# Optimization experiments

Hardware: AMD Instinct MI355X
Metric: run time of the kernel (lower is better)

Reference implementation:

```python
import jax, jax.numpy as jnp
import numpy as np

N = 50_000          # num_nodes
E = 800_000         # num_edges (avg degree 16)
DIMS = [512, 256, 256, 7]   # embedding_dim
SCALING = 2.0


def _glorot(key, shape):
    lim = float(np.sqrt(6.0 / (shape[0] + shape[1])))
    return jax.random.uniform(key, shape, jnp.float32, -lim, lim)


def setup_inputs() -> dict:
    key = jax.random.key(0)
    ks = jax.random.split(key, 16)
    inp = {
        "x": jax.random.normal(ks[0], (N, DIMS[0]), jnp.float32),
        "edge_index": jax.random.randint(ks[1], (2, E), 0, N, dtype=jnp.int32),
        # GCNConv weights (3 layers)
        "W1": _glorot(ks[2], (DIMS[0], DIMS[1])), "b1": jnp.zeros((DIMS[1],), jnp.float32),
        "W2": _glorot(ks[3], (DIMS[1], DIMS[2])), "b2": jnp.zeros((DIMS[2],), jnp.float32),
        "W3": _glorot(ks[4], (DIMS[2], DIMS[3])), "b3": jnp.zeros((DIMS[3],), jnp.float32),
        # pseudo_mlp: Linear(512,512) -> ReLU -> Linear(512,64) -> ReLU -> Linear(64,out)
        "mw1": _glorot(ks[5], (DIMS[0], 512)), "mb1": jnp.zeros((512,), jnp.float32),
        "mw2": _glorot(ks[6], (512, 64)),      "mb2": jnp.zeros((64,), jnp.float32),
        "mw3": _glorot(ks[7], (64, DIMS[-1])), "mb3": jnp.zeros((DIMS[-1],), jnp.float32),
        # parsing_mats[0] (only index 0 is used: learn_soft_edge3 always called with ln=0)
        "parsing0": jnp.ones((DIMS[-1], DIMS[-1]), jnp.float32) / SCALING,
    }
    return inp


def _gcn_conv(h_in, row, col, edge_weight, W, b):
    """PyG-style GCNConv with self-loops, symmetric norm, and per-edge weights."""
    h = h_in @ W                                  # [N, out]
    loop = jnp.arange(N, dtype=row.dtype)
    r = jnp.concatenate([row, loop])
    c = jnp.concatenate([col, loop])
    ew = jnp.concatenate([edge_weight, jnp.ones((N,), h.dtype)])
    deg = jax.ops.segment_sum(ew, c, num_segments=N)
    dinv = jnp.where(deg > 0, jax.lax.rsqrt(jnp.maximum(deg, 1e-12)), 0.0)
    norm = dinv[r] * ew * dinv[c]                 # [E+N]
    out = jax.ops.segment_sum(h[r] * norm[:, None], c, num_segments=N)
    return out + b


def _learn_soft_edge(x, row, col, mw1, mb1, mw2, mb2, mw3, mb3, parsing0):
    # pseudo_mlp logits
    h = jax.nn.relu(x @ mw1 + mb1)
    h = jax.nn.relu(h @ mw2 + mb2)
    logits = h @ mw3 + mb3                        # [N, C]
    s = logits[row]                               # start_logits [E, C]
    e = logits[col]                               # end_logits   [E, C]
    parsing = jax.nn.relu(SCALING * parsing0)     # [C, C]
    # diag(bmm(outer(s,e), P)).sum(-1) == sum_{c,d} s[e,c] * e[e,d] * P[d,c]
    ew = jnp.sum(s * (e @ parsing), axis=1)       # [E]
    mean = ew.mean()
    var = ew.var(ddof=1)                          # torch .var() is unbiased
    return (ew - mean) * jnp.sqrt(1e-4 / var) + 1.0


def reference(x, edge_index, W1, b1, W2, b2, W3, b3,
              mw1, mb1, mw2, mb2, mw3, mb3, parsing0):
    row, col = edge_index[0], edge_index[1]
    ew = _learn_soft_edge(x, row, col, mw1, mb1, mw2, mb2, mw3, mb3, parsing0)
    # layer 0
    h0 = _gcn_conv(x, row, col, ew, W1, b1)       # h = x (saved, pre-ReLU)
    x1 = jax.nn.relu(h0)                          # dropout is identity in eval
    # layer 1 (+ residual to h0)
    x2 = _gcn_conv(x1, row, col, ew, W2, b2)
    x2 = jax.nn.relu(x2) + h0
    # layer 2 (final, no activation)
    out = _gcn_conv(x2, row, col, ew, W3, b3)     # [N, n_classes]
    return out
```

## Files before the change

kernel.cpp:

```cpp
#include <hip/hip_runtime.h>

#define NN 50000
#define EE 800000
#define NB_EDGE 3125
#define NB_E1   1563
#define NB_SCAN 196

typedef __attribute__((ext_vector_type(4))) float f32x4;
typedef __attribute__((ext_vector_type(8))) short bf16x8;
typedef __attribute__((ext_vector_type(8))) unsigned short u16x8;

typedef const __attribute__((address_space(1))) void* gas_p;
typedef __attribute__((address_space(3))) void* las_p;

__device__ __forceinline__ float bf2f(unsigned short u) {
  union { unsigned int i; float f; } v; v.i = ((unsigned int)u) << 16; return v.f;
}
__device__ __forceinline__ unsigned short f2bf(float f) {
  union { float f; unsigned int i; } v; v.f = f;
  unsigned int u = v.i;
  return (unsigned short)((u + 0x7FFFu + ((u >> 16) & 1u)) >> 16);
}

__device__ __forceinline__ int xcd_swizzle(int orig, int nwg) {
  int xcd = orig & 7;
  int pos = orig >> 3;
  int q = nwg >> 3, r = nwg & 7;
  return (xcd < r ? xcd * (q + 1) : r * (q + 1) + (xcd - r) * q) + pos;
}

constexpr size_t O_XBF  = 0;
constexpr size_t O_H1   = O_XBF + 51200000;
constexpr size_t O_G1   = O_H1  + 51200000;
constexpr size_t O_X1   = O_G1  + 25600000;
constexpr size_t O_H2   = O_X1  + 25600000;
constexpr size_t O_LG   = O_H2  + 6400000;
constexpr size_t O_TG   = O_LG  + 1600000;
constexpr size_t O_EWR  = O_TG  + 1600000;
constexpr size_t O_W3P  = O_EWR + 3200000;
constexpr size_t O_RK   = O_W3P + 8192;
constexpr size_t O_CSR  = O_W3P + 3200000;
constexpr size_t O_MW1T = O_CSR + 6400000;
constexpr size_t O_W1T  = O_MW1T + 524288;
constexpr size_t O_W2T  = O_W1T  + 262144;
constexpr size_t O_MW2T = O_W2T  + 131072;
constexpr size_t O_CNT  = O_MW2T + 65536;
constexpr size_t O_RED  = O_CNT  + 200192;
constexpr size_t O_RPT  = O_RED  + 256;
constexpr size_t O_DINV = O_RPT  + 200192;
constexpr size_t O_BSUM = O_DINV + 200192;

__global__ __launch_bounds__(256) void conv_f2bf4(const float* __restrict__ in,
                                                  unsigned short* __restrict__ out, int n4) {
  int i = blockIdx.x * 256 + threadIdx.x;
  if (i >= n4) return;
  const float4 v = ((const float4*)in)[i];
  ushort4 o; o.x = f2bf(v.x); o.y = f2bf(v.y); o.z = f2bf(v.z); o.w = f2bf(v.w);
  ((ushort4*)out)[i] = o;
}

__global__ __launch_bounds__(256)
void conv_weights(const float* __restrict__ mw1, const float* __restrict__ W1,
                  const float* __restrict__ W2, const float* __restrict__ mw2,
                  const float* __restrict__ W3,
                  unsigned short* __restrict__ mw1t, unsigned short* __restrict__ w1t,
                  unsigned short* __restrict__ w2t, unsigned short* __restrict__ mw2t,
                  float* __restrict__ w3p)
{
  int i = blockIdx.x * 256 + threadIdx.x;
  if (i < 262144) {
    int k = i >> 9, n = i & 511;
    mw1t[(size_t)n * 512 + k] = f2bf(mw1[i]);
  } else if (i < 393216) {
    int j = i - 262144, k = j >> 8, n = j & 255;
    w1t[(size_t)n * 512 + k] = f2bf(W1[j]);
  } else if (i < 458752) {
    int j = i - 393216, k = j >> 8, n = j & 255;
    w2t[(size_t)n * 256 + k] = f2bf(W2[j]);
  } else if (i < 491520) {
    int j = i - 458752, k = j >> 6, n = j & 63;
    mw2t[(size_t)n * 512 + k] = f2bf(mw2[j]);
  } else if (i < 493568) {
    int j = i - 491520, d = j >> 3, c = j & 7;
    w3p[j] = (c < 7) ? W3[d * 7 + c] : 0.f;
  }
}

#define GEMM_STAGE(buf, k0)                                                        \
  _Pragma("unroll")                                                                \
  for (int r = 0; r < 4; ++r) {                                                    \
    const int row = r * 32 + wid * 8 + srow8;                                      \
    int ga = bm + row; ga = ga < M_ ? ga : M_ - 1;                                 \
    int gb = bn + row; gb = gb < N_ ? gb : N_ - 1;                                 \
    __builtin_amdgcn_global_load_lds((gas_p)(pA_ + ((size_t)ga * lda_ + (k0)) * 2 + sks * 16), \
                                     (las_p)(ldsA[buf] + row * 64), 16, 0, 0);     \
    __builtin_amdgcn_global_load_lds((gas_p)(pB_ + ((size_t)gb * ldb_ + (k0)) * 2 + sks * 16), \
                                     (las_p)(ldsB[buf] + row * 64), 16, 0, 0);     \
  }

#define GEMM_BODY(A, lda, Bt, ldb_K, M, Ncols, K, bm, bn)                          \
  __shared__ unsigned short ldsA[2][128 * 64];                                     \
  __shared__ unsigned short ldsB[2][128 * 64];                                     \
  const char* pA_ = (const char*)(A);                                              \
  const char* pB_ = (const char*)(Bt);                                             \
  const int lda_ = (lda), ldb_ = (ldb_K), M_ = (M), N_ = (Ncols);                  \
  const int tid  = threadIdx.x;                                                    \
  const int lane = tid & 63;                                                       \
  const int wid  = tid >> 6;                                                       \
  const int wm   = (wid >> 1) << 6;                                                \
  const int wn   = (wid & 1) << 6;                                                 \
  f32x4 acc[4][4] = {};                                                            \
  const int srow8 = lane >> 3;                                                     \
  const int sks   = (lane & 7) ^ srow8;                                            \
  const int nt    = (K) >> 6;                                                      \
  GEMM_STAGE(0, 0)                                                                 \
  for (int t = 0; t < nt; ++t) {                                                   \
    const int cur = t & 1;                                                         \
    if (t + 1 < nt) {                                                              \
      GEMM_STAGE(cur ^ 1, (t + 1) << 6)                                            \
      asm volatile("s_waitcnt vmcnt(8)" ::: "memory");                             \
    } else {                                                                       \
      asm volatile("s_waitcnt vmcnt(0)" ::: "memory");                             \
    }                                                                              \
    __builtin_amdgcn_s_barrier();                                                  \
    __builtin_amdgcn_sched_barrier(0);                                             \
    const int q   = lane >> 4;                                                     \
    const int r15 = lane & 15;                                                     \
    _Pragma("unroll")                                                              \
    for (int kk = 0; kk < 2; ++kk) {                                               \
      bf16x8 af[4], bfr[4];                                                        \
      _Pragma("unroll")                                                            \
      for (int m = 0; m < 4; ++m) {                                                \
        const int ra = wm + m * 16 + r15;                                          \
        af[m]  = *(const bf16x8*)(ldsA[cur] + ra * 64 + (((kk << 2) + q) ^ (ra & 7)) * 8); \
        const int rb = wn + m * 16 + r15;                                          \
        bfr[m] = *(const bf16x8*)(ldsB[cur] + rb * 64 + (((kk << 2) + q) ^ (rb & 7)) * 8); \
      }                                                                            \
      _Pragma("unroll")                                                            \
      for (int m = 0; m < 4; ++m)                                                  \
        _Pragma("unroll")                                                          \
        for (int n = 0; n < 4; ++n)                                                \
          acc[m][n] = __builtin_amdgcn_mfma_f32_16x16x32_bf16(af[m], bfr[n], acc[m][n], 0, 0, 0); \
    }                                                                              \
    __builtin_amdgcn_sched_barrier(0);                                             \
    __builtin_amdgcn_s_barrier();                                                  \
  }

template<bool RELU, bool BIAS>
__global__ __launch_bounds__(256)
void gemm_bf16(const unsigned short* __restrict__ A, int lda,
               const unsigned short* __restrict__ Bt,
               const float* __restrict__ bias,
               unsigned short* __restrict__ C, int ldc,
               int M, int N, int K)
{
  const int nwg  = gridDim.x * gridDim.y;
  const int wgid = xcd_swizzle(blockIdx.y * gridDim.x + blockIdx.x, nwg);
  const int bn   = (wgid % gridDim.x) << 7;
  const int bm   = (wgid / gridDim.x) << 7;

  GEMM_BODY(A, lda, Bt, K, M, N, K, bm, bn)

  const int q   = lane >> 4;
  const int r15 = lane & 15;
#pragma unroll
  for (int m = 0; m < 4; ++m) {
#pragma unroll
    for (int n = 0; n < 4; ++n) {
      const int gc = bn + wn + n * 16 + r15;
#pragma unroll
      for (int i = 0; i < 4; ++i) {
        const int gr = bm + wm + m * 16 + q * 4 + i;
        if (gr < M && gc < N) {
          float f = acc[m][n][i];
          if (BIAS) f += bias[gc];
          if (RELU) f = fmaxf(f, 0.f);
          C[(size_t)gr * ldc + gc] = f2bf(f);
        }
      }
    }
  }
}

__global__ __launch_bounds__(256)
void gemm_fused(const unsigned short* __restrict__ A,
                const unsigned short* __restrict__ Bt,
                const float* __restrict__ mb1,
                unsigned short* __restrict__ h1,
                unsigned short* __restrict__ g1,
                int M)
{
  const int nwg  = gridDim.x * gridDim.y;
  const int wgid = xcd_swizzle(blockIdx.y * gridDim.x + blockIdx.x, nwg);
  const int bnt  = wgid % gridDim.x;
  const int bn   = bnt << 7;
  const int bm   = (wgid / gridDim.x) << 7;

  GEMM_BODY(A, 512, Bt, 512, M, 768, 512, bm, bn)

  const int q   = lane >> 4;
  const int r15 = lane & 15;
  if (bnt < 4) {
#pragma unroll
    for (int m = 0; m < 4; ++m) {
#pragma unroll
      for (int n = 0; n < 4; ++n) {
        const int gc = bn + wn + n * 16 + r15;
        const float b = mb1[gc];
#pragma unroll
        for (int i = 0; i < 4; ++i) {
          const int gr = bm + wm + m * 16 + q * 4 + i;
          if (gr < M) h1[(size_t)gr * 512 + gc] = f2bf(fmaxf(acc[m][n][i] + b, 0.f));
        }
      }
    }
  } else {
#pragma unroll
    for (int m = 0; m < 4; ++m) {
#pragma unroll
      for (int n = 0; n < 4; ++n) {
        const int gc = bn - 512 + wn + n * 16 + r15;
#pragma unroll
        for (int i = 0; i < 4; ++i) {
          const int gr = bm + wm + m * 16 + q * 4 + i;
          if (gr < M) g1[(size_t)gr * 256 + gc] = f2bf(acc[m][n][i]);
        }
      }
    }
  }
}

__global__ __launch_bounds__(256)
void logits_kernel(const unsigned short* __restrict__ h2, const float* __restrict__ mw3,
                   const float* __restrict__ mb3, const float* __restrict__ par,
                   float* __restrict__ Lg, float* __restrict__ Tg)
{
  __shared__ float w[64 * 8];
  __shared__ float P[64];
  int tid = threadIdx.x;
  for (int i = tid; i < 512; i += 256) {
    int k = i >> 3, c = i & 7;
    w[i] = (c < 7) ? mw3[k * 7 + c] : 0.f;
  }
  if (tid < 64) {
    int d = tid >> 3, c = tid & 7;
    P[tid] = (d < 7 && c < 7) ? fmaxf(2.0f * par[d * 7 + c], 0.f) : 0.f;
  }
  __syncthreads();
  int n = blockIdx.x * 256 + tid;
  if (n >= NN) return;
  const unsigned short* hr = h2 + (size_t)n * 64;
  f32x4 L0 = {0,0,0,0}, L1 = {0,0,0,0};
  for (int k = 0; k < 64; k += 4) {
    ushort4 v = *(const ushort4*)(hr + k);
    float xs[4] = {bf2f(v.x), bf2f(v.y), bf2f(v.z), bf2f(v.w)};
#pragma unroll
    for (int j = 0; j < 4; ++j) {
      L0 += xs[j] * *(const f32x4*)&w[(k + j) * 8];
      L1 += xs[j] * *(const f32x4*)&w[(k + j) * 8 + 4];
    }
  }
  float Ls[8] = {L0[0], L0[1], L0[2], L0[3], L1[0], L1[1], L1[2], 0.f};
#pragma unroll
  for (int c = 0; c < 7; ++c) Ls[c] += mb3[c];
  f32x4 T0 = {0,0,0,0}, T1 = {0,0,0,0};
#pragma unroll
  for (int d = 0; d < 7; ++d) {
    T0 += Ls[d] * *(const f32x4*)&P[d * 8];
    T1 += Ls[d] * *(const f32x4*)&P[d * 8 + 4];
  }
  f32x4 o0 = {Ls[0], Ls[1], Ls[2], Ls[3]};
  f32x4 o1 = {Ls[4], Ls[5], Ls[6], 0.f};
  *(f32x4*)(Lg + (size_t)n * 8)     = o0;
  *(f32x4*)(Lg + (size_t)n * 8 + 4) = o1;
  *(f32x4*)(Tg + (size_t)n * 8)     = T0;
  *(f32x4*)(Tg + (size_t)n * 8 + 4) = T1;
}

__global__ __launch_bounds__(256)
void edge1_kernel(const int* __restrict__ row, const int* __restrict__ col,
                  const float* __restrict__ Lg, const float* __restrict__ Tg,
                  float* __restrict__ ew_raw, int* __restrict__ cnt,
                  unsigned short* __restrict__ rk, double* __restrict__ part)
{
  __shared__ double shs[4], shs2[4];
  const int e0 = blockIdx.x * 512 + threadIdx.x;
  const int e1 = e0 + 256;
  double s = 0.0, s2 = 0.0;
  if (e1 < EE) {
    int r0 = row[e0], c0 = col[e0];
    int r1 = row[e1], c1 = col[e1];
    float4 a00 = *(const float4*)(Lg + (size_t)r0 * 8);
    float4 a01 = *(const float4*)(Lg + (size_t)r0 * 8 + 4);
    float4 a10 = *(const float4*)(Lg + (size_t)r1 * 8);
    float4 a11 = *(const float4*)(Lg + (size_t)r1 * 8 + 4);
    float4 b00 = *(const float4*)(Tg + (size_t)c0 * 8);
    float4 b01 = *(const float4*)(Tg + (size_t)c0 * 8 + 4);
    float4 b10 = *(const float4*)(Tg + (size_t)c1 * 8);
    float4 b11 = *(const float4*)(Tg + (size_t)c1 * 8 + 4);
    float v0 = a00.x*b00.x + a00.y*b00.y + a00.z*b00.z + a00.w*b00.w
             + a01.x*b01.x + a01.y*b01.y + a01.z*b01.z + a01.w*b01.w;
    float v1 = a10.x*b10.x + a10.y*b10.y + a10.z*b10.z + a10.w*b10.w
             + a11.x*b11.x + a11.y*b11.y + a11.z*b11.z + a11.w*b11.w;
    ew_raw[e0] = v0; ew_raw[e1] = v1;
    int p0 = atomicAdd(&cnt[c0], 1);
    int p1 = atomicAdd(&cnt[c1], 1);
    rk[e0] = (unsigned short)p0;
    rk[e1] = (unsigned short)p1;
    s = (double)v0 + (double)v1;
    s2 = (double)v0 * (double)v0 + (double)v1 * (double)v1;
  } else if (e0 < EE) {
    int r0 = row[e0], c0 = col[e0];
    float4 a00 = *(const float4*)(Lg + (size_t)r0 * 8);
    float4 a01 = *(const float4*)(Lg + (size_t)r0 * 8 + 4);
    float4 b00 = *(const float4*)(Tg + (size_t)c0 * 8);
    float4 b01 = *(const float4*)(Tg + (size_t)c0 * 8 + 4);
    float v0 = a00.x*b00.x + a00.y*b00.y + a00.z*b00.z + a00.w*b00.w
             + a01.x*b01.x + a01.y*b01.y + a01.z*b01.z + a01.w*b01.w;
    ew_raw[e0] = v0;
    int p0 = atomicAdd(&cnt[c0], 1);
    rk[e0] = (unsigned short)p0;
    s = (double)v0; s2 = (double)v0 * (double)v0;
  }
  for (int off = 32; off; off >>= 1) {
    s  += __shfl_down(s, off);
    s2 += __shfl_down(s2, off);
  }
  int wv = threadIdx.x >> 6;
  if ((threadIdx.x & 63) == 0) { shs[wv] = s; shs2[wv] = s2; }
  __syncthreads();
  if (threadIdx.x == 0) {
    part[blockIdx.x]         = shs[0] + shs[1] + shs[2] + shs[3];
    part[NB_E1 + blockIdx.x] = shs2[0] + shs2[1] + shs2[2] + shs2[3];
  }
}

__global__ __launch_bounds__(1024)
void redpart_kernel(const double* __restrict__ part, double* __restrict__ red)
{
  __shared__ double sh[16][2];
  int tid = threadIdx.x;
  double s = 0.0, s2 = 0.0;
  for (int i = tid; i < NB_E1; i += 1024) {
    s  += part[i];
    s2 += part[NB_E1 + i];
  }
  for (int off = 32; off; off >>= 1) {
    s  += __shfl_down(s, off);
    s2 += __shfl_down(s2, off);
  }
  if ((tid & 63) == 0) { sh[tid >> 6][0] = s; sh[tid >> 6][1] = s2; }
  __syncthreads();
  if (tid == 0) {
    double a = 0.0, b = 0.0;
    for (int i = 0; i < 16; ++i) { a += sh[i][0]; b += sh[i][1]; }
    red[0] = a; red[1] = b;
  }
}

__global__ __launch_bounds__(256)
void edge2_kernel(const int* __restrict__ row, const int* __restrict__ col,
                  const float* __restrict__ ew_raw, const unsigned short* __restrict__ rk,
                  const double* __restrict__ red, const int* __restrict__ rowptr,
                  int2* __restrict__ csr_sw)
{
  int e = blockIdx.x * 256 + threadIdx.x;
  if (e >= EE) return;
  double mean = red[0] / (double)EE;
  double var  = (red[1] - (double)EE * mean * mean) / (double)(EE - 1);
  double scl  = sqrt(1e-4 / var);
  float v = (float)(((double)ew_raw[e] - mean) * scl) + 1.0f;
  int r = row[e], c = col[e];
  int2 sw; sw.x = r; sw.y = __float_as_int(v);
  csr_sw[rowptr[c] + (int)rk[e]] = sw;
}

__global__ __launch_bounds__(256)
void degdinv_kernel(const int* __restrict__ rowptr, const int2* __restrict__ csr_sw,
                    float* __restrict__ dinv)
{
  int n = blockIdx.x * 256 + threadIdx.x;
  if (n >= NN) return;
  int s = rowptr[n], e = rowptr[n + 1];
  float deg = 0.f;
  for (int i = s; i < e; ++i) deg += __int_as_float(csr_sw[i].y);
  float d = deg + 1.0f;
  dinv[n] = d > 0.f ? 1.0f / sqrtf(fmaxf(d, 1e-12f)) : 0.f;
}

__global__ __launch_bounds__(256)
void scale_csr_kernel(int2* __restrict__ csr_sw, const float* __restrict__ dinv)
{
  int i = blockIdx.x * 256 + threadIdx.x;
  if (i >= EE) return;
  int2 sw = csr_sw[i];
  sw.y = __float_as_int(__int_as_float(sw.y) * dinv[sw.x]);
  csr_sw[i] = sw;
}

__global__ __launch_bounds__(256)
void scan1_kernel(const int* __restrict__ cnt, int* __restrict__ bsum)
{
  __shared__ int sh[4];
  int i = blockIdx.x * 256 + threadIdx.x;
  int v = (i < NN) ? cnt[i] : 0;
  for (int off = 32; off; off >>= 1) v += __shfl_down(v, off);
  if ((threadIdx.x & 63) == 0) sh[threadIdx.x >> 6] = v;
  __syncthreads();
  if (threadIdx.x == 0) bsum[blockIdx.x] = sh[0] + sh[1] + sh[2] + sh[3];
}

__global__ __launch_bounds__(256)
void scan2_kernel(int* __restrict__ bsum)
{
  __shared__ int sh[256];
  int tid = threadIdx.x;
  int v = (tid < NB_SCAN) ? bsum[tid] : 0;
  sh[tid] = v;
  __syncthreads();
  for (int off = 1; off < 256; off <<= 1) {
    int t = (tid >= off) ? sh[tid - off] : 0;
    __syncthreads();
    sh[tid] += t;
    __syncthreads();
  }
  if (tid < NB_SCAN) bsum[tid] = sh[tid] - v;
}

__global__ __launch_bounds__(256)
void scan3_kernel(const int* __restrict__ cnt, const int* __restrict__ bsum,
                  int* __restrict__ rowptr)
{
  __shared__ int sh[256];
  int tid = threadIdx.x;
  int i = blockIdx.x * 256 + tid;
  int v = (i < NN) ? cnt[i] : 0;
  sh[tid] = v;
  __syncthreads();
  for (int off = 1; off < 256; off <<= 1) {
    int t = (tid >= off) ? sh[tid - off] : 0;
    __syncthreads();
    sh[tid] += t;
    __syncthreads();
  }
  if (i < NN) rowptr[i + 1] = bsum[blockIdx.x] + sh[tid];
  if (i == 0) rowptr[0] = 0;
}

#define AGG_ACC(sw_, v_)                                                     \
  {                                                                          \
    float w_ = __int_as_float((sw_).y);                                      \
    a0 += w_ * bf2f((v_)[0]); a1 += w_ * bf2f((v_)[1]);                      \
    a2 += w_ * bf2f((v_)[2]); a3 += w_ * bf2f((v_)[3]);                      \
    a4 += w_ * bf2f((v_)[4]); a5 += w_ * bf2f((v_)[5]);                      \
    a6 += w_ * bf2f((v_)[6]); a7 += w_ * bf2f((v_)[7]);                      \
  }

template<int MODE>
__global__ __launch_bounds__(256)
void agg256_kernel(const int* __restrict__ rowptr, const int2* __restrict__ csr_sw,
                   const unsigned short* __restrict__ gsrc,
                   const float* __restrict__ dinv, const float* __restrict__ bias,
                   const unsigned short* __restrict__ h0in,
                   unsigned short* __restrict__ h0out,
                   unsigned short* __restrict__ xout,
                   const float* __restrict__ w3p, float* __restrict__ y3)
{
  const int tid = threadIdx.x;
  const int hw  = tid >> 5;
  const int l5  = tid & 31;
  const size_t colbase = (size_t)(l5 << 3);
  const int stride = (int)gridDim.x * 8;

  for (int n = blockIdx.x * 8 + hw; n < NN; n += stride) {
    const int dbase = l5 << 3;
    const float dn = dinv[n];
    u16x8 sv = *(const u16x8*)(gsrc + (size_t)n * 256 + dbase);
    float4 b0 = *(const float4*)(bias + dbase);
    float4 b1 = *(const float4*)(bias + dbase + 4);
    float a0=0,a1=0,a2=0,a3=0,a4=0,a5=0,a6=0,a7=0;
    const int s = rowptr[n], e = rowptr[n + 1];
    int i = s;
    for (; i + 7 < e; i += 8) {
      int2 sw[8];
#pragma unroll
      for (int u = 0; u < 8; ++u) sw[u] = csr_sw[i + u];
      u16x8 v[8];
#pragma unroll
      for (int u = 0; u < 8; ++u) v[u] = *(const u16x8*)(gsrc + (size_t)sw[u].x * 256 + colbase);
#pragma unroll
      for (int u = 0; u < 8; ++u) AGG_ACC(sw[u], v[u])
    }
    for (; i + 3 < e; i += 4) {
      int2 sw[4];
#pragma unroll
      for (int u = 0; u < 4; ++u) sw[u] = csr_sw[i + u];
      u16x8 v[4];
#pragma unroll
      for (int u = 0; u < 4; ++u) v[u] = *(const u16x8*)(gsrc + (size_t)sw[u].x * 256 + colbase);
#pragma unroll
      for (int u = 0; u < 4; ++u) AGG_ACC(sw[u], v[u])
    }
    for (; i < e; ++i) {
      int2 sw = csr_sw[i];
      u16x8 v = *(const u16x8*)(gsrc + (size_t)sw.x * 256 + colbase);
      AGG_ACC(sw, v)
    }
    const float wd = dn * dn;
    float f0 = dn * a0 + wd * bf2f(sv[0]) + b0.x;
    float f1 = dn * a1 + wd * bf2f(sv[1]) + b0.y;
    float f2 = dn * a2 + wd * bf2f(sv[2]) + b0.z;
    float f3 = dn * a3 + wd * bf2f(sv[3]) + b0.w;
    float f4 = dn * a4 + wd * bf2f(sv[4]) + b1.x;
    float f5 = dn * a5 + wd * bf2f(sv[5]) + b1.y;
    float f6 = dn * a6 + wd * bf2f(sv[6]) + b1.z;
    float f7 = dn * a7 + wd * bf2f(sv[7]) + b1.w;
    const size_t o = (size_t)n * 256 + dbase;
    if (MODE == 0) {
      u16x8 h;
      h[0] = f2bf(f0); h[1] = f2bf(f1); h[2] = f2bf(f2); h[3] = f2bf(f3);
      h[4] = f2bf(f4); h[5] = f2bf(f5); h[6] = f2bf(f6); h[7] = f2bf(f7);
      *(u16x8*)(h0out + o) = h;
      u16x8 xo;
      xo[0] = f2bf(fmaxf(f0, 0.f)); xo[1] = f2bf(fmaxf(f1, 0.f));
      xo[2] = f2bf(fmaxf(f2, 0.f)); xo[3] = f2bf(fmaxf(f3, 0.f));
      xo[4] = f2bf(fmaxf(f4, 0.f)); xo[5] = f2bf(fmaxf(f5, 0.f));
      xo[6] = f2bf(fmaxf(f6, 0.f)); xo[7] = f2bf(fmaxf(f7, 0.f));
      *(u16x8*)(xout + o) = xo;
    } else {
      u16x8 h = *(const u16x8*)(h0in + o);
      float xv0 = bf2f(f2bf(fmaxf(f0, 0.f) + bf2f(h[0])));
      float xv1 = bf2f(f2bf(fmaxf(f1, 0.f) + bf2f(h[1])));
      float xv2 = bf2f(f2bf(fmaxf(f2, 0.f) + bf2f(h[2])));
      float xv3 = bf2f(f2bf(fmaxf(f3, 0.f) + bf2f(h[3])));
      float xv4 = bf2f(f2bf(fmaxf(f4, 0.f) + bf2f(h[4])));
      float xv5 = bf2f(f2bf(fmaxf(f5, 0.f) + bf2f(h[5])));
      float xv6 = bf2f(f2bf(fmaxf(f6, 0.f) + bf2f(h[6])));
      float xv7 = bf2f(f2bf(fmaxf(f7, 0.f) + bf2f(h[7])));
      const float* w3r = w3p + (size_t)dbase * 8;
      f32x4 p0 = {0,0,0,0}, p1 = {0,0,0,0};
      p0 += xv0 * *(const f32x4*)(w3r +  0); p1 += xv0 * *(const f32x4*)(w3r +  4);
      p0 += xv1 * *(const f32x4*)(w3r +  8); p1 += xv1 * *(const f32x4*)(w3r + 12);
      p0 += xv2 * *(const f32x4*)(w3r + 16); p1 += xv2 * *(const f32x4*)(w3r + 20);
      p0 += xv3 * *(const f32x4*)(w3r + 24); p1 += xv3 * *(const f32x4*)(w3r + 28);
      p0 += xv4 * *(const f32x4*)(w3r + 32); p1 += xv4 * *(const f32x4*)(w3r + 36);
      p0 += xv5 * *(const f32x4*)(w3r + 40); p1 += xv5 * *(const f32x4*)(w3r + 44);
      p0 += xv6 * *(const f32x4*)(w3r + 48); p1 += xv6 * *(const f32x4*)(w3r + 52);
      p0 += xv7 * *(const f32x4*)(w3r + 56); p1 += xv7 * *(const f32x4*)(w3r + 60);
#pragma unroll
      for (int off = 1; off < 32; off <<= 1) {
        p0[0] += __shfl_xor(p0[0], off); p0[1] += __shfl_xor(p0[1], off);
        p0[2] += __shfl_xor(p0[2], off); p0[3] += __shfl_xor(p0[3], off);
        p1[0] += __shfl_xor(p1[0], off); p1[1] += __shfl_xor(p1[1], off);
        p1[2] += __shfl_xor(p1[2], off); p1[3] += __shfl_xor(p1[3], off);
      }
      if (l5 == 0) {
        *(f32x4*)(y3 + (size_t)n * 8)     = p0;
        *(f32x4*)(y3 + (size_t)n * 8 + 4) = p1;
      }
    }
  }
}

__global__ __launch_bounds__(256)
void agg7_kernel(const int* __restrict__ rowptr, const int2* __restrict__ csr_sw,
                 const float* __restrict__ y3,
                 const float* __restrict__ dinv, const float* __restrict__ b3,
                 float* __restrict__ out)
{
  int n = blockIdx.x * 32 + (threadIdx.x >> 3);
  if (n >= NN) return;
  int j = threadIdx.x & 7;
  float acc = 0.f;
  int s = rowptr[n], e = rowptr[n + 1];
  int i = s;
  for (; i + 3 < e; i += 4) {
    int2 sw0 = csr_sw[i],     sw1 = csr_sw[i + 1];
    int2 sw2 = csr_sw[i + 2], sw3 = csr_sw[i + 3];
    float v0 = y3[(size_t)sw0.x * 8 + j];
    float v1 = y3[(size_t)sw1.x * 8 + j];
    float v2 = y3[(size_t)sw2.x * 8 + j];
    float v3 = y3[(size_t)sw3.x * 8 + j];
    acc += __int_as_float(sw0.y) * v0 + __int_as_float(sw1.y) * v1
         + __int_as_float(sw2.y) * v2 + __int_as_float(sw3.y) * v3;
  }
  for (; i < e; ++i) {
    int2 sw = csr_sw[i];
    acc += __int_as_float(sw.y) * y3[(size_t)sw.x * 8 + j];
  }
  float dn = dinv[n];
  acc = dn * acc + dn * dn * y3[(size_t)n * 8 + j];
  if (j < 7) out[(size_t)n * 7 + j] = acc + b3[j];
}

extern "C" void kernel_launch(void* const* d_in, const int* in_sizes, int n_in,
                              void* d_out, int out_size, void* d_ws, size_t ws_size,
                              hipStream_t stream)
{
  const float* x   = (const float*)d_in[0];
  const int*   ei  = (const int*)d_in[1];
  const float* W1  = (const float*)d_in[2];
  const float* b1  = (const float*)d_in[3];
  const float* W2  = (const float*)d_in[4];
  const float* b2  = (const float*)d_in[5];
  const float* W3  = (const float*)d_in[6];
  const float* b3  = (const float*)d_in[7];
  const float* mw1 = (const float*)d_in[8];
  const float* mb1 = (const float*)d_in[9];
  const float* mw2 = (const float*)d_in[10];
  const float* mb2 = (const float*)d_in[11];
  const float* mw3 = (const float*)d_in[12];
  const float* mb3 = (const float*)d_in[13];
  const float* par = (const float*)d_in[14];
  const int* row = ei;
  const int* col = ei + EE;
  float* out = (float*)d_out;

  char* ws = (char*)d_ws;
  unsigned short* x_bf  = (unsigned short*)(ws + O_XBF);
  unsigned short* h0    = (unsigned short*)(ws + O_XBF);
  unsigned short* h1_bf = (unsigned short*)(ws + O_H1);
  unsigned short* g2_bf = (unsigned short*)(ws + O_H1);
  unsigned short* g1_bf = (unsigned short*)(ws + O_G1);
  unsigned short* x1_bf = (unsigned short*)(ws + O_X1);
  unsigned short* h2_bf = (unsigned short*)(ws + O_H2);
  float* Lg      = (float*)(ws + O_LG);
  float* Tg      = (float*)(ws + O_TG);
  float* ew_raw  = (float*)(ws + O_EWR);
  float* y3      = (float*)(ws + O_EWR);
  float* w3p     = (float*)(ws + O_W3P);
  unsigned short* rk = (unsigned short*)(ws + O_RK);
  int2*  csr_sw  = (int2*)(ws + O_CSR);
  double* part   = (double*)(ws + O_CSR);
  unsigned short* mw1t = (unsigned short*)(ws + O_MW1T);
  unsigned short* w1t  = (unsigned short*)(ws + O_W1T);
  unsigned short* w2t  = (unsigned short*)(ws + O_W2T);
  unsigned short* mw2t = (unsigned short*)(ws + O_MW2T);
  int*    cnt    = (int*)(ws + O_CNT);
  double* red    = (double*)(ws + O_RED);
  int*    rowptr = (int*)(ws + O_RPT);
  float*  dinv   = (float*)(ws + O_DINV);
  int*    bsum   = (int*)(ws + O_BSUM);

  hipMemsetAsync(ws + O_CNT, 0, 200192, stream);

  conv_f2bf4<<<25000, 256, 0, stream>>>(x, x_bf, NN * 512 / 4);
  conv_weights<<<1929, 256, 0, stream>>>(mw1, W1, W2, mw2, W3, mw1t, w1t, w2t, mw2t, w3p);

  gemm_fused<<<dim3(6, 391), 256, 0, stream>>>(x_bf, mw1t, mb1, h1_bf, g1_bf, NN);
  gemm_bf16<true,  true ><<<dim3(1, 391), 256, 0, stream>>>(h1_bf, 512, mw2t, mb2, h2_bf, 64, NN, 64, 512);
  logits_kernel<<<196, 256, 0, stream>>>(h2_bf, mw3, mb3, par, Lg, Tg);

  edge1_kernel<<<NB_E1, 256, 0, stream>>>(row, col, Lg, Tg, ew_raw, cnt, rk, part);
  redpart_kernel<<<1, 1024, 0, stream>>>(part, red);
  scan1_kernel<<<NB_SCAN, 256, 0, stream>>>(cnt, bsum);
  scan2_kernel<<<1, 256, 0, stream>>>(bsum);
  scan3_kernel<<<NB_SCAN, 256, 0, stream>>>(cnt, bsum, rowptr);
  edge2_kernel<<<NB_EDGE, 256, 0, stream>>>(row, col, ew_raw, rk, red, rowptr, csr_sw);
  degdinv_kernel<<<196, 256, 0, stream>>>(rowptr, csr_sw, dinv);
  scale_csr_kernel<<<NB_EDGE, 256, 0, stream>>>(csr_sw, dinv);

  agg256_kernel<0><<<1536, 256, 0, stream>>>(rowptr, csr_sw, g1_bf, dinv, b1, nullptr, h0, x1_bf, nullptr, nullptr);
  gemm_bf16<false, false><<<dim3(2, 391), 256, 0, stream>>>(x1_bf, 256, w2t, nullptr, g2_bf, 256, NN, 256, 256);
  agg256_kernel<1><<<1536, 256, 0, stream>>>(rowptr, csr_sw, g2_bf, dinv, b2, h0, nullptr, nullptr, w3p, y3);
  agg7_kernel<<<1563, 256, 0, stream>>>(rowptr, csr_sw, y3, dinv, b3, out);
}
```

Measured before the change: 377.2 us.

## Fuse MLP second GEMM with logits projection and widen edge1 per-thread work

Replaces the separate 512->64 GEMM and the logits kernel with one MFMA kernel that computes the 64-wide hidden layer in registers, then applies ReLU, the 64->7 projection with a lane shuffle reduction, and the parsing-matrix transform before writing Lg/Tg. This removes the h2 round trip through global memory and one launch. Separately, edge1 now processes four edges per thread with the gathers batched, so fewer blocks are launched and more loads are in flight per thread. The 128x64 tile with 2x4 MFMA per wave gives small per-block work and more shuffle reductions in the epilogue.

```diff
diff --git a/kernel.cpp b/kernel.cpp
--- a/kernel.cpp
+++ b/kernel.cpp
@@ -3,7 +3,7 @@
 #define NN 50000
 #define EE 800000
 #define NB_EDGE 3125
-#define NB_E1   1563
+#define NB_E1   782
 #define NB_SCAN 196
 
 typedef __attribute__((ext_vector_type(4))) float f32x4;
@@ -39,6 +39,7 @@
 constexpr size_t O_EWR  = O_TG  + 1600000;
 constexpr size_t O_W3P  = O_EWR + 3200000;
 constexpr size_t O_RK   = O_W3P + 8192;
+constexpr size_t O_MW3P = O_RK  + 1600000;
 constexpr size_t O_CSR  = O_W3P + 3200000;
 constexpr size_t O_MW1T = O_CSR + 6400000;
 constexpr size_t O_W1T  = O_MW1T + 524288;
@@ -62,10 +63,10 @@
 __global__ __launch_bounds__(256)
 void conv_weights(const float* __restrict__ mw1, const float* __restrict__ W1,
                   const float* __restrict__ W2, const float* __restrict__ mw2,
-                  const float* __restrict__ W3,
+                  const float* __restrict__ W3, const float* __restrict__ mw3,
                   unsigned short* __restrict__ mw1t, unsigned short* __restrict__ w1t,
                   unsigned short* __restrict__ w2t, unsigned short* __restrict__ mw2t,
-                  float* __restrict__ w3p)
+                  float* __restrict__ w3p, float* __restrict__ mw3p)
 {
   int i = blockIdx.x * 256 + threadIdx.x;
   if (i < 262144) {
@@ -83,6 +84,9 @@
   } else if (i < 493568) {
     int j = i - 491520, d = j >> 3, c = j & 7;
     w3p[j] = (c < 7) ? W3[d * 7 + c] : 0.f;
+  } else if (i < 494080) {
+    int j = i - 493568, d = j >> 3, c = j & 7;
+    mw3p[j] = (c < 7) ? mw3[d * 7 + c] : 0.f;
   }
 }
 
@@ -231,50 +235,127 @@
 }
 
 __global__ __launch_bounds__(256)
-void logits_kernel(const unsigned short* __restrict__ h2, const float* __restrict__ mw3,
-                   const float* __restrict__ mb3, const float* __restrict__ par,
-                   float* __restrict__ Lg, float* __restrict__ Tg)
-{
-  __shared__ float w[64 * 8];
-  __shared__ float P[64];
-  int tid = threadIdx.x;
-  for (int i = tid; i < 512; i += 256) {
-    int k = i >> 3, c = i & 7;
-    w[i] = (c < 7) ? mw3[k * 7 + c] : 0.f;
-  }
+void mlp2_logits_kernel(const unsigned short* __restrict__ A,
+                        const unsigned short* __restrict__ Bt,
+                        const float* __restrict__ mb2,
+                        const float* __restrict__ mw3p,
+                        const float* __restrict__ mb3,
+                        const float* __restrict__ par,
+                        float* __restrict__ Lg, float* __restrict__ Tg,
+                        int M)
+{
+  __shared__ unsigned short ldsA[2][128 * 64];
+  __shared__ unsigned short ldsB[2][64 * 64];
+  __shared__ float Psh[64];
+  const int tid  = threadIdx.x;
+  const int lane = tid & 63;
+  const int wid  = tid >> 6;
+  const int bm   = blockIdx.x << 7;
+  f32x4 acc[2][4] = {};
+  const int srow8 = lane >> 3;
+  const int sks   = (lane & 7) ^ srow8;
+
   if (tid < 64) {
     int d = tid >> 3, c = tid & 7;
-    P[tid] = (d < 7 && c < 7) ? fmaxf(2.0f * par[d * 7 + c], 0.f) : 0.f;
-  }
-  __syncthreads();
-  int n = blockIdx.x * 256 + tid;
-  if (n >= NN) return;
-  const unsigned short* hr = h2 + (size_t)n * 64;
-  f32x4 L0 = {0,0,0,0}, L1 = {0,0,0,0};
-  for (int k = 0; k < 64; k += 4) {
-    ushort4 v = *(const ushort4*)(hr + k);
-    float xs[4] = {bf2f(v.x), bf2f(v.y), bf2f(v.z), bf2f(v.w)};
-#pragma unroll
-    for (int j = 0; j < 4; ++j) {
-      L0 += xs[j] * *(const f32x4*)&w[(k + j) * 8];
-      L1 += xs[j] * *(const f32x4*)&w[(k + j) * 8 + 4];
-    }
-  }
-  float Ls[8] = {L0[0], L0[1], L0[2], L0[3], L1[0], L1[1], L1[2], 0.f};
-#pragma unroll
-  for (int c = 0; c < 7; ++c) Ls[c] += mb3[c];
-  f32x4 T0 = {0,0,0,0}, T1 = {0,0,0,0};
-#pragma unroll
-  for (int d = 0; d < 7; ++d) {
-    T0 += Ls[d] * *(const f32x4*)&P[d * 8];
-    T1 += Ls[d] * *(const f32x4*)&P[d * 8 + 4];
-  }
-  f32x4 o0 = {Ls[0], Ls[1], Ls[2], Ls[3]};
-  f32x4 o1 = {Ls[4], Ls[5], Ls[6], 0.f};
-  *(f32x4*)(Lg + (size_t)n * 8)     = o0;
-  *(f32x4*)(Lg + (size_t)n * 8 + 4) = o1;
-  *(f32x4*)(Tg + (size_t)n * 8)     = T0;
-  *(f32x4*)(Tg + (size_t)n * 8 + 4) = T1;
+    Psh[tid] = (d < 7 && c < 7) ? fmaxf(2.0f * par[d * 7 + c], 0.f) : 0.f;
+  }
+
+#define M2_STAGE(buf, k0)                                                          \
+  _Pragma("unroll")                                                                \
+  for (int r = 0; r < 4; ++r) {                                                    \
+    const int rowA = r * 32 + wid * 8 + srow8;                                     \
+    int ga = bm + rowA; ga = ga < M ? ga : M - 1;                                  \
+    __builtin_amdgcn_global_load_lds((gas_p)((const char*)A + ((size_t)ga * 512 + (k0)) * 2 + sks * 16), \
+                                     (las_p)(ldsA[buf] + rowA * 64), 16, 0, 0);    \
+  }                                                                                \
+  _Pragma("unroll")                                                                \
+  for (int r = 0; r < 2; ++r) {                                                    \
+    const int rowB = r * 32 + wid * 8 + srow8;                                     \
+    __builtin_amdgcn_global_load_lds((gas_p)((const char*)Bt + ((size_t)rowB * 512 + (k0)) * 2 + sks * 16), \
+                                     (las_p)(ldsB[buf] + rowB * 64), 16, 0, 0);    \
+  }
+
+  M2_STAGE(0, 0)
+  for (int t = 0; t < 8; ++t) {
+    const int cur = t & 1;
+    if (t < 7) {
+      M2_STAGE(cur ^ 1, (t + 1) << 6)
+      asm volatile("s_waitcnt vmcnt(6)" ::: "memory");
+    } else {
+      asm volatile("s_waitcnt vmcnt(0)" ::: "memory");
+    }
+    __builtin_amdgcn_s_barrier();
+    __builtin_amdgcn_sched_barrier(0);
+    const int q   = lane >> 4;
+    const int r15 = lane & 15;
+#pragma unroll
+    for (int kk = 0; kk < 2; ++kk) {
+      bf16x8 af[2], bfr[4];
+#pragma unroll
+      for (int m = 0; m < 2; ++m) {
+        const int ra = wid * 32 + m * 16 + r15;
+        af[m] = *(const bf16x8*)(ldsA[cur] + ra * 64 + (((kk << 2) + q) ^ (ra & 7)) * 8);
+      }
+#pragma unroll
+      for (int n = 0; n < 4; ++n) {
+        const int rb = n * 16 + r15;
+        bfr[n] = *(const bf16x8*)(ldsB[cur] + rb * 64 + (((kk << 2) + q) ^ (rb & 7)) * 8);
+      }
+#pragma unroll
+      for (int m = 0; m < 2; ++m)
+#pragma unroll
+        for (int n = 0; n < 4; ++n)
+          acc[m][n] = __builtin_amdgcn_mfma_f32_16x16x32_bf16(af[m], bfr[n], acc[m][n], 0, 0, 0);
+    }
+    __builtin_amdgcn_sched_barrier(0);
+    __builtin_amdgcn_s_barrier();
+  }
+
+  const int q   = lane >> 4;
+  const int r15 = lane & 15;
+#pragma unroll
+  for (int m = 0; m < 2; ++m) {
+#pragma unroll
+    for (int i = 0; i < 4; ++i) {
+      f32x4 Llo = {0,0,0,0}, Lhi = {0,0,0,0};
+#pragma unroll
+      for (int n = 0; n < 4; ++n) {
+        const int colB = n * 16 + r15;
+        float h2v = fmaxf(acc[m][n][i] + mb2[colB], 0.f);
+        Llo += h2v * *(const f32x4*)(mw3p + colB * 8);
+        Lhi += h2v * *(const f32x4*)(mw3p + colB * 8 + 4);
+      }
+#pragma unroll
+      for (int off = 1; off < 16; off <<= 1) {
+        Llo[0] += __shfl_xor(Llo[0], off); Llo[1] += __shfl_xor(Llo[1], off);
+        Llo[2] += __shfl_xor(Llo[2], off); Llo[3] += __shfl_xor(Llo[3], off);
+        Lhi[0] += __shfl_xor(Lhi[0], off); Lhi[1] += __shfl_xor(Lhi[1], off);
+        Lhi[2] += __shfl_xor(Lhi[2], off); Lhi[3] += __shfl_xor(Lhi[3], off);
+      }
+      if (r15 == 0) {
+        const int grow = bm + wid * 32 + m * 16 + q * 4 + i;
+        if (grow < M) {
+          float Ls[8];
+          Ls[0] = Llo[0] + mb3[0]; Ls[1] = Llo[1] + mb3[1];
+          Ls[2] = Llo[2] + mb3[2]; Ls[3] = Llo[3] + mb3[3];
+          Ls[4] = Lhi[0] + mb3[4]; Ls[5] = Lhi[1] + mb3[5];
+          Ls[6] = Lhi[2] + mb3[6]; Ls[7] = 0.f;
+          f32x4 T0 = {0,0,0,0}, T1 = {0,0,0,0};
+#pragma unroll
+          for (int d = 0; d < 7; ++d) {
+            T0 += Ls[d] * *(const f32x4*)&Psh[d * 8];
+            T1 += Ls[d] * *(const f32x4*)&Psh[d * 8 + 4];
+          }
+          f32x4 o0 = {Ls[0], Ls[1], Ls[2], Ls[3]};
+          f32x4 o1 = {Ls[4], Ls[5], Ls[6], 0.f};
+          *(f32x4*)(Lg + (size_t)grow * 8)     = o0;
+          *(f32x4*)(Lg + (size_t)grow * 8 + 4) = o1;
+          *(f32x4*)(Tg + (size_t)grow * 8)     = T0;
+          *(f32x4*)(Tg + (size_t)grow * 8 + 4) = T1;
+        }
+      }
+    }
+  }
 }
 
 __global__ __launch_bounds__(256)
@@ -284,43 +365,30 @@
                   unsigned short* __restrict__ rk, double* __restrict__ part)
 {
   __shared__ double shs[4], shs2[4];
-  const int e0 = blockIdx.x * 512 + threadIdx.x;
-  const int e1 = e0 + 256;
+  const int base = blockIdx.x * 1024 + threadIdx.x;
   double s = 0.0, s2 = 0.0;
-  if (e1 < EE) {
-    int r0 = row[e0], c0 = col[e0];
-    int r1 = row[e1], c1 = col[e1];
-    float4 a00 = *(const float4*)(Lg + (size_t)r0 * 8);
-    float4 a01 = *(const float4*)(Lg + (size_t)r0 * 8 + 4);
-    float4 a10 = *(const float4*)(Lg + (size_t)r1 * 8);
-    float4 a11 = *(const float4*)(Lg + (size_t)r1 * 8 + 4);
-    float4 b00 = *(const float4*)(Tg + (size_t)c0 * 8);
-    float4 b01 = *(const float4*)(Tg + (size_t)c0 * 8 + 4);
-    float4 b10 = *(const float4*)(Tg + (size_t)c1 * 8);
-    float4 b11 = *(const float4*)(Tg + (size_t)c1 * 8 + 4);
-    float v0 = a00.x*b00.x + a00.y*b00.y + a00.z*b00.z + a00.w*b00.w
-             + a01.x*b01.x + a01.y*b01.y + a01.z*b01.z + a01.w*b01.w;
-    float v1 = a10.x*b10.x + a10.y*b10.y + a10.z*b10.z + a10.w*b10.w
-             + a11.x*b11.x + a11.y*b11.y + a11.z*b11.z + a11.w*b11.w;
-    ew_raw[e0] = v0; ew_raw[e1] = v1;
-    int p0 = atomicAdd(&cnt[c0], 1);
-    int p1 = atomicAdd(&cnt[c1], 1);
-    rk[e0] = (unsigned short)p0;
-    rk[e1] = (unsigned short)p1;
-    s = (double)v0 + (double)v1;
-    s2 = (double)v0 * (double)v0 + (double)v1 * (double)v1;
-  } else if (e0 < EE) {
-    int r0 = row[e0], c0 = col[e0];
-    float4 a00 = *(const float4*)(Lg + (size_t)r0 * 8);
-    float4 a01 = *(const float4*)(Lg + (size_t)r0 * 8 + 4);
-    float4 b00 = *(const float4*)(Tg + (size_t)c0 * 8);
-    float4 b01 = *(const float4*)(Tg + (size_t)c0 * 8 + 4);
-    float v0 = a00.x*b00.x + a00.y*b00.y + a00.z*b00.z + a00.w*b00.w
-             + a01.x*b01.x + a01.y*b01.y + a01.z*b01.z + a01.w*b01.w;
-    ew_raw[e0] = v0;
-    int p0 = atomicAdd(&cnt[c0], 1);
-    rk[e0] = (unsigned short)p0;
-    s = (double)v0; s2 = (double)v0 * (double)v0;
+  int idx[4]; bool ok[4];
+#pragma unroll
+  for (int u = 0; u < 4; ++u) { idx[u] = base + u * 256; ok[u] = idx[u] < EE; }
+  int r[4], c[4];
+#pragma unroll
+  for (int u = 0; u < 4; ++u) if (ok[u]) { r[u] = row[idx[u]]; c[u] = col[idx[u]]; }
+  float4 A0[4], A1[4], B0[4], B1[4];
+#pragma unroll
+  for (int u = 0; u < 4; ++u) if (ok[u]) {
+    A0[u] = *(const float4*)(Lg + (size_t)r[u] * 8);
+    A1[u] = *(const float4*)(Lg + (size_t)r[u] * 8 + 4);
+    B0[u] = *(const float4*)(Tg + (size_t)c[u] * 8);
+    B1[u] = *(const float4*)(Tg + (size_t)c[u] * 8 + 4);
+  }
+#pragma unroll
+  for (int u = 0; u < 4; ++u) if (ok[u]) {
+    float v = A0[u].x*B0[u].x + A0[u].y*B0[u].y + A0[u].z*B0[u].z + A0[u].w*B0[u].w
+            + A1[u].x*B1[u].x + A1[u].y*B1[u].y + A1[u].z*B1[u].z + A1[u].w*B1[u].w;
+    ew_raw[idx[u]] = v;
+    int p = atomicAdd(&cnt[c[u]], 1);
+    rk[idx[u]] = (unsigned short)p;
+    s += (double)v; s2 += (double)v * (double)v;
   }
   for (int off = 32; off; off >>= 1) {
     s  += __shfl_down(s, off);
@@ -623,13 +691,13 @@
   unsigned short* g2_bf = (unsigned short*)(ws + O_H1);
   unsigned short* g1_bf = (unsigned short*)(ws + O_G1);
   unsigned short* x1_bf = (unsigned short*)(ws + O_X1);
-  unsigned short* h2_bf = (unsigned short*)(ws + O_H2);
   float* Lg      = (float*)(ws + O_LG);
   float* Tg      = (float*)(ws + O_TG);
   float* ew_raw  = (float*)(ws + O_EWR);
   float* y3      = (float*)(ws + O_EWR);
   float* w3p     = (float*)(ws + O_W3P);
   unsigned short* rk = (unsigned short*)(ws + O_RK);
+  float* mw3p    = (float*)(ws + O_MW3P);
   int2*  csr_sw  = (int2*)(ws + O_CSR);
   double* part   = (double*)(ws + O_CSR);
   unsigned short* mw1t = (unsigned short*)(ws + O_MW1T);
@@ -645,11 +713,10 @@
   hipMemsetAsync(ws + O_CNT, 0, 200192, stream);
 
   conv_f2bf4<<<25000, 256, 0, stream>>>(x, x_bf, NN * 512 / 4);
-  conv_weights<<<1929, 256, 0, stream>>>(mw1, W1, W2, mw2, W3, mw1t, w1t, w2t, mw2t, w3p);
+  conv_weights<<<1930, 256, 0, stream>>>(mw1, W1, W2, mw2, W3, mw3, mw1t, w1t, w2t, mw2t, w3p, mw3p);
 
   gemm_fused<<<dim3(6, 391), 256, 0, stream>>>(x_bf, mw1t, mb1, h1_bf, g1_bf, NN);
-  gemm_bf16<true,  true ><<<dim3(1, 391), 256, 0, stream>>>(h1_bf, 512, mw2t, mb2, h2_bf, 64, NN, 64, 512);
-  logits_kernel<<<196, 256, 0, stream>>>(h2_bf, mw3, mb3, par, Lg, Tg);
+  mlp2_logits_kernel<<<391, 256, 0, stream>>>(h1_bf, mw2t, mb2, mw3p, mb3, par, Lg, Tg, NN);
 
   edge1_kernel<<<NB_E1, 256, 0, stream>>>(row, col, Lg, Tg, ew_raw, cnt, rk, part);
   redpart_kernel<<<1, 1024, 0, stream>>>(part, red);
```

After: 371.9 us. No clear change (-1.4%).
